# Performance work log

Hardware: AMD Instinct MI355X
Metric: run time of the kernel (lower is better)

Reference implementation:

```python
import jax, jax.numpy as jnp
import numpy as np

T = 500        # num_target
R = 50         # num_resource
NS = 1000      # hard-coded sample count in the torch loop
F_STATE = 2    # raw state features; num_feature = F_STATE + T = 502
NOISE_F = 2
H1, H2 = 32, 16
NEG_SLOPE = 0.2


def _lrelu(x):
    return jnp.where(x >= 0, x, NEG_SLOPE * x)


def setup_inputs() -> dict:
    key = jax.random.key(0)
    ks = jax.random.split(key, 16)
    d = {}
    d["state"] = jax.random.normal(ks[0], (1, T, F_STATE), jnp.float32)
    d["def_cur_loc"] = jax.random.uniform(ks[1], (R, T), jnp.float32)
    d["feat_noise"] = jax.random.uniform(ks[2], (1, T, NOISE_F), jnp.float32)
    d["gumbel_u"] = jax.random.uniform(ks[3], (NS, R, T), jnp.float32, 1e-6, 1.0 - 1e-6)
    # learned / fixed parameters
    d["payoff"] = jax.random.normal(ks[4], (T, T), jnp.float32)
    # row-normalized adjacency surrogate
    a = jax.random.uniform(ks[5], (T, T), jnp.float32)
    d["norm_adj"] = a / jnp.sum(a, axis=1, keepdims=True)
    fin = F_STATE + T + NOISE_F  # 504 = num_feature + noise_feat
    d["gc1_w"] = jax.random.normal(ks[6], (fin, H1), jnp.float32) / np.sqrt(fin)
    d["gc1_b"] = jnp.zeros((H1,), jnp.float32)
    d["gc2_w"] = jax.random.normal(ks[7], (H1, H2), jnp.float32) / np.sqrt(H1)
    d["gc2_b"] = jnp.zeros((H2,), jnp.float32)
    d["bn_gamma"] = jnp.ones((T,), jnp.float32)
    d["bn_beta"] = jnp.zeros((T,), jnp.float32)
    d["actgen_w"] = jax.random.normal(ks[8], (H2 * T, T), jnp.float32) / np.sqrt(H2 * T)
    d["actgen_v"] = jax.random.normal(ks[9], (T, T), jnp.float32) / np.sqrt(T)
    return d


def reference(state, def_cur_loc, feat_noise, gumbel_u, payoff, norm_adj,
              gc1_w, gc1_b, gc2_w, gc2_b, bn_gamma, bn_beta,
              actgen_w, actgen_v):
    # x = cat(state, payoff, noise) -> (1, T, 504)
    x = jnp.concatenate([state, payoff[None], feat_noise], axis=2)

    def gcn(h, w, b):  # GraphConvolution: norm_adj @ (h @ w) + b
        return jnp.einsum('tu,buc->btc', norm_adj, h @ w) + b

    def bn(h):  # BatchNorm1d(T) in eval mode (running mean 0, var 1)
        return h * bn_gamma[None, :, None] + bn_beta[None, :, None]

    h = _lrelu(bn(gcn(x, gc1_w, gc1_b)))          # (1, T, 32); dropout is eval-mode identity
    h = _lrelu(bn(gcn(h, gc2_w, gc2_b)))          # (1, T, 16)
    xf = h.reshape(H2 * T)                        # x.view(-1, 16*T).squeeze()

    # act_gen: shared linear head + location projection -> per-resource logits (R, T)
    logits = xf @ actgen_w + def_cur_loc @ actgen_v

    # 1000 independent stochastic samples (the torch for-loop, fully batched):
    g = -jnp.log(-jnp.log(gumbel_u))              # (NS, R, T) gumbel noise
    act_estimates = jax.nn.softmax(logits[None] + g, axis=-1)  # (1000, R, T)
    # state_value head exists in the module but is not returned; omitted.
    return act_estimates
```

## Files before the change

kernel.cpp:

```cpp
#include <hip/hip_runtime.h>

#define T_ 500
#define R_ 50
#define NS_ 1000
#define H1_ 32
#define H2_ 16
#define NEG_ 0.2f
#define NROWS_ (NS_ * R_)

__device__ __forceinline__ float lrelu(float x) { return x >= 0.f ? x : NEG_ * x; }

__device__ __forceinline__ float wave_sum_dpp(float x) {
    int t;
    t = __builtin_amdgcn_update_dpp(0, __float_as_int(x), 0x111, 0xf, 0xf, true);
    x += __int_as_float(t);
    t = __builtin_amdgcn_update_dpp(0, __float_as_int(x), 0x112, 0xf, 0xf, true);
    x += __int_as_float(t);
    t = __builtin_amdgcn_update_dpp(0, __float_as_int(x), 0x114, 0xf, 0xf, true);
    x += __int_as_float(t);
    t = __builtin_amdgcn_update_dpp(0, __float_as_int(x), 0x118, 0xf, 0xf, true);
    x += __int_as_float(t);
    t = __builtin_amdgcn_update_dpp(0, __float_as_int(x), 0x142, 0xf, 0xf, true);
    x += __int_as_float(t);
    t = __builtin_amdgcn_update_dpp(0, __float_as_int(x), 0x143, 0xf, 0xf, true);
    x += __int_as_float(t);
    return __int_as_float(__builtin_amdgcn_readlane(__float_as_int(x), 63));
}

__global__ __launch_bounds__(256) void k1_xw(const float* __restrict__ state,
                                             const float* __restrict__ payoff,
                                             const float* __restrict__ noise,
                                             const float* __restrict__ w,
                                             float* __restrict__ y1) {
    __shared__ float xs[504];
    __shared__ float red[8][H1_];
    int t = blockIdx.x, tid = threadIdx.x;
    for (int u = tid; u < T_; u += 256) xs[2 + u] = payoff[t * T_ + u];
    if (tid == 0) {
        xs[0] = state[t * 2];     xs[1] = state[t * 2 + 1];
        xs[502] = noise[t * 2];   xs[503] = noise[t * 2 + 1];
    }
    __syncthreads();
    int c = tid & 31, kg = tid >> 5;
    float acc = 0.f;
#pragma unroll 7
    for (int f = kg; f < 504; f += 8) acc += xs[f] * w[f * H1_ + c];
    red[kg][c] = acc;
    __syncthreads();
    if (tid < H1_) {
        float a = 0.f;
#pragma unroll
        for (int s = 0; s < 8; ++s) a += red[s][tid];
        y1[t * H1_ + tid] = a;
    }
}

__global__ __launch_bounds__(256) void k2_adj_fused(const float* __restrict__ adj,
                                                    const float* __restrict__ y1,
                                                    const float* __restrict__ b,
                                                    const float* __restrict__ gamma,
                                                    const float* __restrict__ beta,
                                                    const float* __restrict__ w2,
                                                    float* __restrict__ y2) {
    __shared__ float arow[T_];
    __shared__ float red[8][H1_];
    __shared__ float h1row[H1_];
    int t = blockIdx.x, tid = threadIdx.x;
    for (int u = tid; u < T_; u += 256) arow[u] = adj[t * T_ + u];
    __syncthreads();
    int c = tid & 31, kg = tid >> 5;
    float acc = 0.f;
#pragma unroll 4
    for (int u = kg; u < T_; u += 8) acc += arow[u] * y1[u * H1_ + c];
    red[kg][c] = acc;
    __syncthreads();
    if (tid < H1_) {
        float a = 0.f;
#pragma unroll
        for (int s = 0; s < 8; ++s) a += red[s][tid];
        h1row[tid] = lrelu((a + b[tid]) * gamma[t] + beta[t]);
    }
    __syncthreads();
    if (tid < H2_) {
        float a = 0.f;
#pragma unroll
        for (int cc = 0; cc < H1_; ++cc) a += h1row[cc] * w2[cc * H2_ + tid];
        y2[t * H2_ + tid] = a;
    }
}

__global__ __launch_bounds__(256) void k3_adj2_aw(const float* __restrict__ adj,
                                                  const float* __restrict__ y2,
                                                  const float* __restrict__ b2,
                                                  const float* __restrict__ gamma,
                                                  const float* __restrict__ beta,
                                                  const float* __restrict__ aw,
                                                  float* __restrict__ part1) {
    __shared__ float arow[T_];
    __shared__ float red[16][H2_];
    __shared__ float xfr[H2_];
    int t = blockIdx.x, tid = threadIdx.x;
    for (int u = tid; u < T_; u += 256) arow[u] = adj[t * T_ + u];
    __syncthreads();
    int c2 = tid & 15, kg = tid >> 4;
    float acc = 0.f;
#pragma unroll 4
    for (int u = kg; u < T_; u += 16) acc += arow[u] * y2[u * H2_ + c2];
    red[kg][c2] = acc;
    __syncthreads();
    if (tid < H2_) {
        float a = 0.f;
#pragma unroll
        for (int s = 0; s < 16; ++s) a += red[s][tid];
        xfr[tid] = lrelu((a + b2[tid]) * gamma[t] + beta[t]);
    }
    __syncthreads();
    float acc0 = 0.f, acc1 = 0.f;
#pragma unroll
    for (int c = 0; c < H2_; ++c) {
        float xv = xfr[c];
        const float* awr = aw + (t * H2_ + c) * T_;
        acc0 += xv * awr[tid];
        if (tid < T_ - 256) acc1 += xv * awr[256 + tid];
    }
    part1[t * T_ + tid] = acc0;
    if (tid < T_ - 256) part1[t * T_ + 256 + tid] = acc1;
}

__global__ __launch_bounds__(256) void k4_logits_part(const float* __restrict__ dloc,
                                                      const float* __restrict__ av,
                                                      const float* __restrict__ part1,
                                                      float* __restrict__ part2) {
    int r = blockIdx.x;
    int jb = blockIdx.y & 1, q = blockIdx.y >> 1;
    __shared__ float drow[125];
    int tid = threadIdx.x;
    int t0 = q * 125;
    if (tid < 125) drow[tid] = dloc[r * T_ + t0 + tid];
    __syncthreads();
    if (tid >= 250) return;
    int j = jb * 250 + tid;
    float acc = 0.f;
#pragma unroll 5
    for (int i = 0; i < 125; ++i) {
        int t = t0 + i;
        acc += drow[i] * av[t * T_ + j] + part1[t * T_ + j];
    }
    part2[q * (R_ * T_) + r * T_ + j] = acc;
}

__global__ __launch_bounds__(256) void k4_reduce_exp(const float* __restrict__ part2,
                                                     float* __restrict__ elog) {
    int gid = blockIdx.x * 256 + threadIdx.x;
    if (gid >= R_ * T_) return;
    float v = part2[gid] + part2[R_ * T_ + gid] +
              part2[2 * R_ * T_ + gid] + part2[3 * R_ * T_ + gid];
    elog[gid] = __expf(v);
}

__global__ __launch_bounds__(256) void k7_softmax(const float4* __restrict__ gu,
                                                  const float4* __restrict__ elog,
                                                  float4* __restrict__ out) {
    int wave = threadIdx.x >> 6;
    int lane = threadIdx.x & 63;
    int row = blockIdx.x * 4 + wave;
    int r = row % R_;
    const float4* grow = gu + (size_t)row * 125;
    const float4* erow = elog + r * 125;
    bool has1 = lane < 61;

    float4 g0 = grow[lane];
    float4 e0 = erow[lane];
    float4 g1, e1;
    if (has1) {
        g1 = grow[64 + lane];
        e1 = erow[64 + lane];
    }
    float p[8];
    p[0] = e0.x * __builtin_amdgcn_rcpf(-__log2f(g0.x));
    p[1] = e0.y * __builtin_amdgcn_rcpf(-__log2f(g0.y));
    p[2] = e0.z * __builtin_amdgcn_rcpf(-__log2f(g0.z));
    p[3] = e0.w * __builtin_amdgcn_rcpf(-__log2f(g0.w));
    if (has1) {
        p[4] = e1.x * __builtin_amdgcn_rcpf(-__log2f(g1.x));
        p[5] = e1.y * __builtin_amdgcn_rcpf(-__log2f(g1.y));
        p[6] = e1.z * __builtin_amdgcn_rcpf(-__log2f(g1.z));
        p[7] = e1.w * __builtin_amdgcn_rcpf(-__log2f(g1.w));
    } else {
        p[4] = p[5] = p[6] = p[7] = 0.f;
    }
    float s = ((p[0] + p[1]) + (p[2] + p[3])) + ((p[4] + p[5]) + (p[6] + p[7]));
    float tot = wave_sum_dpp(s);
    float inv = __builtin_amdgcn_rcpf(tot);

    float4* orow = out + (size_t)row * 125;
    float4 o0 = {p[0] * inv, p[1] * inv, p[2] * inv, p[3] * inv};
    orow[lane] = o0;
    if (has1) {
        float4 o1 = {p[4] * inv, p[5] * inv, p[6] * inv, p[7] * inv};
        orow[64 + lane] = o1;
    }
}

extern "C" void kernel_launch(void* const* d_in, const int* in_sizes, int n_in,
                              void* d_out, int out_size, void* d_ws, size_t ws_size,
                              hipStream_t stream) {
    const float* state  = (const float*)d_in[0];
    const float* dloc   = (const float*)d_in[1];
    const float* noise  = (const float*)d_in[2];
    const float* gu     = (const float*)d_in[3];
    const float* payoff = (const float*)d_in[4];
    const float* adj    = (const float*)d_in[5];
    const float* g1w    = (const float*)d_in[6];
    const float* g1b    = (const float*)d_in[7];
    const float* g2w    = (const float*)d_in[8];
    const float* g2b    = (const float*)d_in[9];
    const float* gamma  = (const float*)d_in[10];
    const float* beta   = (const float*)d_in[11];
    const float* aw     = (const float*)d_in[12];
    const float* av     = (const float*)d_in[13];
    float* out = (float*)d_out;

    float* ws     = (float*)d_ws;
    float* y1     = ws;
    float* y2     = ws + 16000;
    float* part1  = ws + 24000;
    float* part2  = ws + 274000;
    float* elog   = ws + 374000;

    k1_xw<<<T_, 256, 0, stream>>>(state, payoff, noise, g1w, y1);
    k2_adj_fused<<<T_, 256, 0, stream>>>(adj, y1, g1b, gamma, beta, g2w, y2);
    k3_adj2_aw<<<T_, 256, 0, stream>>>(adj, y2, g2b, gamma, beta, aw, part1);
    k4_logits_part<<<dim3(R_, 8), 256, 0, stream>>>(dloc, av, part1, part2);
    k4_reduce_exp<<<(R_ * T_ + 255) / 256, 256, 0, stream>>>(part2, elog);
    k7_softmax<<<NROWS_ / 4, 256, 0, stream>>>(
        (const float4*)gu, (const float4*)elog, (float4*)out);
}
```

Baseline: 71.61 us.

## Split fused softmax into separate row-sum and normalize kernels

Splits the single-pass gumbel-softmax kernel into two kernels. The first reads the gumbel noise and computes each row's inverse sum. The second rereads the noise, recomputes the terms and writes the normalized output. This may separate the read phase from the write phase so each streams more cleanly. In exchange it reads the 100MB gumbel tensor twice, adds a launch and a workspace buffer, and repeats the log and reciprocal work.

```diff
diff --git a/kernel.cpp b/kernel.cpp
--- a/kernel.cpp
+++ b/kernel.cpp
@@ -158,11 +158,10 @@
     elog[gid] = __expf(v);
 }
 
-__global__ __launch_bounds__(256) void k7_softmax(const float4* __restrict__ gu,
-                                                  const float4* __restrict__ elog,
-                                                  float4* __restrict__ out) {
-    int wave = threadIdx.x >> 6;
-    int lane = threadIdx.x & 63;
+__global__ __launch_bounds__(256) void k7a_sums(const float4* __restrict__ gu,
+                                                const float4* __restrict__ elog,
+                                                float* __restrict__ invsum) {
+    int wave = threadIdx.x >> 6, lane = threadIdx.x & 63;
     int row = blockIdx.x * 4 + wave;
     int r = row % R_;
     const float4* grow = gu + (size_t)row * 125;
@@ -172,32 +171,54 @@
     float4 g0 = grow[lane];
     float4 e0 = erow[lane];
     float4 g1, e1;
+    if (has1) { g1 = grow[64 + lane]; e1 = erow[64 + lane]; }
+
+    float p0 = e0.x * __builtin_amdgcn_rcpf(-__log2f(g0.x));
+    float p1 = e0.y * __builtin_amdgcn_rcpf(-__log2f(g0.y));
+    float p2 = e0.z * __builtin_amdgcn_rcpf(-__log2f(g0.z));
+    float p3 = e0.w * __builtin_amdgcn_rcpf(-__log2f(g0.w));
+    float p4 = 0.f, p5 = 0.f, p6 = 0.f, p7 = 0.f;
     if (has1) {
-        g1 = grow[64 + lane];
-        e1 = erow[64 + lane];
-    }
-    float p[8];
-    p[0] = e0.x * __builtin_amdgcn_rcpf(-__log2f(g0.x));
-    p[1] = e0.y * __builtin_amdgcn_rcpf(-__log2f(g0.y));
-    p[2] = e0.z * __builtin_amdgcn_rcpf(-__log2f(g0.z));
-    p[3] = e0.w * __builtin_amdgcn_rcpf(-__log2f(g0.w));
-    if (has1) {
-        p[4] = e1.x * __builtin_amdgcn_rcpf(-__log2f(g1.x));
-        p[5] = e1.y * __builtin_amdgcn_rcpf(-__log2f(g1.y));
-        p[6] = e1.z * __builtin_amdgcn_rcpf(-__log2f(g1.z));
-        p[7] = e1.w * __builtin_amdgcn_rcpf(-__log2f(g1.w));
-    } else {
-        p[4] = p[5] = p[6] = p[7] = 0.f;
-    }
-    float s = ((p[0] + p[1]) + (p[2] + p[3])) + ((p[4] + p[5]) + (p[6] + p[7]));
+        p4 = e1.x * __builtin_amdgcn_rcpf(-__log2f(g1.x));
+        p5 = e1.y * __builtin_amdgcn_rcpf(-__log2f(g1.y));
+        p6 = e1.z * __builtin_amdgcn_rcpf(-__log2f(g1.z));
+        p7 = e1.w * __builtin_amdgcn_rcpf(-__log2f(g1.w));
+    }
+    float s = ((p0 + p1) + (p2 + p3)) + ((p4 + p5) + (p6 + p7));
     float tot = wave_sum_dpp(s);
-    float inv = __builtin_amdgcn_rcpf(tot);
+    if (lane == 0) invsum[row] = __builtin_amdgcn_rcpf(tot);
+}
+
+__global__ __launch_bounds__(256) void k7b_norm(const float4* __restrict__ gu,
+                                                const float4* __restrict__ elog,
+                                                const float* __restrict__ invsum,
+                                                float4* __restrict__ out) {
+    int wave = threadIdx.x >> 6, lane = threadIdx.x & 63;
+    int row = blockIdx.x * 4 + wave;
+    int r = row % R_;
+    bool has1 = lane < 61;
+
+    float inv = invsum[row];
+    const float4* grow = gu + (size_t)row * 125;
+    const float4* erow = elog + r * 125;
+    float4 g0 = grow[lane];
+    float4 e0 = erow[lane];
+    float4 g1, e1;
+    if (has1) { g1 = grow[64 + lane]; e1 = erow[64 + lane]; }
 
     float4* orow = out + (size_t)row * 125;
-    float4 o0 = {p[0] * inv, p[1] * inv, p[2] * inv, p[3] * inv};
+    float4 o0;
+    o0.x = e0.x * __builtin_amdgcn_rcpf(-__log2f(g0.x)) * inv;
+    o0.y = e0.y * __builtin_amdgcn_rcpf(-__log2f(g0.y)) * inv;
+    o0.z = e0.z * __builtin_amdgcn_rcpf(-__log2f(g0.z)) * inv;
+    o0.w = e0.w * __builtin_amdgcn_rcpf(-__log2f(g0.w)) * inv;
     orow[lane] = o0;
     if (has1) {
-        float4 o1 = {p[4] * inv, p[5] * inv, p[6] * inv, p[7] * inv};
+        float4 o1;
+        o1.x = e1.x * __builtin_amdgcn_rcpf(-__log2f(g1.x)) * inv;
+        o1.y = e1.y * __builtin_amdgcn_rcpf(-__log2f(g1.y)) * inv;
+        o1.z = e1.z * __builtin_amdgcn_rcpf(-__log2f(g1.z)) * inv;
+        o1.w = e1.w * __builtin_amdgcn_rcpf(-__log2f(g1.w)) * inv;
         orow[64 + lane] = o1;
     }
 }
@@ -227,12 +248,15 @@
     float* part1  = ws + 24000;
     float* part2  = ws + 274000;
     float* elog   = ws + 374000;
+    float* invsum = ws + 400000;
 
     k1_xw<<<T_, 256, 0, stream>>>(state, payoff, noise, g1w, y1);
     k2_adj_fused<<<T_, 256, 0, stream>>>(adj, y1, g1b, gamma, beta, g2w, y2);
     k3_adj2_aw<<<T_, 256, 0, stream>>>(adj, y2, g2b, gamma, beta, aw, part1);
     k4_logits_part<<<dim3(R_, 8), 256, 0, stream>>>(dloc, av, part1, part2);
     k4_reduce_exp<<<(R_ * T_ + 255) / 256, 256, 0, stream>>>(part2, elog);
-    k7_softmax<<<NROWS_ / 4, 256, 0, stream>>>(
-        (const float4*)gu, (const float4*)elog, (float4*)out);
-}
+    k7a_sums<<<NROWS_ / 4, 256, 0, stream>>>(
+        (const float4*)gu, (const float4*)elog, invsum);
+    k7b_norm<<<NROWS_ / 4, 256, 0, stream>>>(
+        (const float4*)gu, (const float4*)elog, invsum, (float4*)out);
+}
```

Result: slower. 86.48 us (+20.8%).
